# Performance work log

Hardware: AMD Instinct MI355X
Metric: run time of the kernel (lower is better)

Reference implementation:

```python
import jax, jax.numpy as jnp
import numpy as np

B, S, D, H = 4, 2048, 1024, 16
HD = D // H  # head_dim = 64


def setup_inputs() -> dict:
    key = jax.random.key(0)
    ks = jax.random.split(key, 5)
    scale = 0.02
    x = jax.random.normal(ks[0], (B, S, D), dtype=jnp.float32)
    W_qkv = jax.random.normal(ks[1], (D, 3 * D), dtype=jnp.float32) * scale
    b_qkv = jnp.zeros((3 * D,), dtype=jnp.float32)
    W_out = jax.random.normal(ks[2], (D, D), dtype=jnp.float32) * scale
    b_out = jnp.zeros((D,), dtype=jnp.float32)
    return {"x": x, "W_qkv": W_qkv, "b_qkv": b_qkv, "W_out": W_out, "b_out": b_out}


def reference(x, W_qkv, b_qkv, W_out, b_out):
    b, s, d = x.shape
    qkv = x @ W_qkv + b_qkv                      # [B,S,3D]
    q, k, v = jnp.split(qkv, 3, axis=-1)
    # [B,S,D] -> [B,H,S,hd]
    q = q.reshape(b, s, H, HD).transpose(0, 2, 1, 3)
    k = k.reshape(b, s, H, HD).transpose(0, 2, 1, 3)
    v = v.reshape(b, s, H, HD).transpose(0, 2, 1, 3)
    scores = jnp.einsum('bhqd,bhkd->bhqk', q, k) / jnp.sqrt(jnp.float32(HD))
    causal = jnp.tril(jnp.ones((s, s), dtype=bool))  # [S,S]
    scores = jnp.where(causal[None, None], scores, -jnp.inf)
    probs = jax.nn.softmax(scores, axis=-1)
    # dropout is identity in eval mode
    attn = jnp.einsum('bhqk,bhkd->bhqd', probs, v)  # [B,H,S,hd]
    attn = attn.transpose(0, 2, 1, 3).reshape(b, s, d)
    return attn @ W_out + b_out
```

## Files before the change

### kernel.cpp

```cpp
#include <hip/hip_runtime.h>


typedef short s16;
typedef __attribute__((ext_vector_type(4))) short s16x4;
typedef __attribute__((ext_vector_type(8))) short bf16x8;
typedef __attribute__((ext_vector_type(4))) float f32x4;

__device__ __forceinline__ s16 f2bf(float f) {
    union { float f; unsigned int i; } v;
    v.f = f;
    unsigned int r = v.i + 0x7fffu + ((v.i >> 16) & 1u);
    return (s16)(r >> 16);
}

__device__ __forceinline__ void load_lds16(const s16* g, s16* lds_base) {
    __builtin_amdgcn_global_load_lds(
        (const __attribute__((address_space(1))) void*)g,
        (__attribute__((address_space(3))) void*)lds_base, 16, 0, 0);
}

__global__ void cast_f32_bf16(const float* __restrict__ in, s16* __restrict__ out) {
    const int i = (blockIdx.x * 256 + threadIdx.x) * 4;
    const float4 f = *(const float4*)(in + i);
    s16x4 r = {f2bf(f.x), f2bf(f.y), f2bf(f.z), f2bf(f.w)};
    *(s16x4*)(out + i) = r;
}

__global__ void transpose_cast(const float* __restrict__ in,
                               s16* __restrict__ out, int R, int C) {
    __shared__ float tile[32][33];
    const int cb = blockIdx.x * 32, rb = blockIdx.y * 32;
    const int tx = threadIdx.x, ty = threadIdx.y;
#pragma unroll
    for (int i = 0; i < 32; i += 8)
        tile[ty + i][tx] = in[(size_t)(rb + ty + i) * C + cb + tx];
    __syncthreads();
#pragma unroll
    for (int i = 0; i < 32; i += 8)
        out[(size_t)(cb + ty + i) * R + rb + tx] = f2bf(tile[tx][ty + i]);
}

template <bool OUT_F32>
__global__ __launch_bounds__(256) void gemm_bt_bias(
    const s16* __restrict__ A,
    const s16* __restrict__ Bt,
    const float* __restrict__ bias,
    void* __restrict__ Cv,
    int M, int N, int K) {
    __shared__ __attribute__((aligned(16))) s16 As[128 * 32];
    __shared__ __attribute__((aligned(16))) s16 Bs[128 * 32];

    const int tid  = threadIdx.x;
    const int lane = tid & 63;
    const int wave = tid >> 6;
    const int l15  = lane & 15;
    const int quad = lane >> 4;
    const int m0 = blockIdx.y * 128;
    const int n0 = blockIdx.x * 128;
    const int wm = (wave & 1) * 64;
    const int wn = (wave >> 1) * 64;

    f32x4 acc[4][4];
#pragma unroll
    for (int i = 0; i < 4; ++i)
#pragma unroll
        for (int j = 0; j < 4; ++j)
            acc[i][j] = (f32x4){0.f, 0.f, 0.f, 0.f};

    const int r_a = tid >> 2;
    const int kp  = tid & 3;

    for (int k0 = 0; k0 < K; k0 += 32) {
        __syncthreads();
#pragma unroll
        for (int c = 0; c < 2; ++c) {
            load_lds16(A  + (size_t)(m0 + c * 64 + r_a) * K + k0 + kp * 8, As + c * 2048 + wave * 512);
            load_lds16(Bt + (size_t)(n0 + c * 64 + r_a) * K + k0 + kp * 8, Bs + c * 2048 + wave * 512);
        }
        __syncthreads();

        bf16x8 af[4], bfv[4];
#pragma unroll
        for (int mt = 0; mt < 4; ++mt)
            af[mt] = *(const bf16x8*)(As + (wm + mt * 16 + l15) * 32 + quad * 8);
#pragma unroll
        for (int nt = 0; nt < 4; ++nt)
            bfv[nt] = *(const bf16x8*)(Bs + (wn + nt * 16 + l15) * 32 + quad * 8);
#pragma unroll
        for (int mt = 0; mt < 4; ++mt)
#pragma unroll
            for (int nt = 0; nt < 4; ++nt)
                acc[mt][nt] = __builtin_amdgcn_mfma_f32_16x16x32_bf16(af[mt], bfv[nt], acc[mt][nt], 0, 0, 0);
    }

#pragma unroll
    for (int nt = 0; nt < 4; ++nt) {
        const int col = n0 + wn + nt * 16 + l15;
        const float bv = bias[col];
#pragma unroll
        for (int mt = 0; mt < 4; ++mt) {
            const int rowb = m0 + wm + mt * 16 + quad * 4;
#pragma unroll
            for (int r = 0; r < 4; ++r) {
                const float v = acc[mt][nt][r] + bv;
                if constexpr (OUT_F32)
                    ((float*)Cv)[(size_t)(rowb + r) * N + col] = v;
                else
                    ((s16*)Cv)[(size_t)(rowb + r) * N + col] = f2bf(v);
            }
        }
    }
}

__global__ __launch_bounds__(256) void attn_fwd(
    const s16* __restrict__ qkv,
    s16* __restrict__ attn) {
    __shared__ __attribute__((aligned(16))) s16 Ks[64 * 72];
    __shared__ __attribute__((aligned(16))) s16 Vt[64 * 72];
    __shared__ __attribute__((aligned(16))) s16 Ps[4][2][16][72];

    const int tid  = threadIdx.x;
    const int lane = tid & 63;
    const int wave = tid >> 6;
    const int l15  = lane & 15;
    const int quad = lane >> 4;
    const int bh = blockIdx.y;
    const size_t rowbase = (size_t)(bh >> 4) * 2048;
    const int hoff = (bh & 15) * 64;
    const int r_s = tid >> 3;
    const int p_s = tid & 7;

    const float C2 = 0.18033688011112042f;
    const float M2 = 12.0f;

#pragma unroll
    for (int phase = 0; phase < 2; ++phase) {
        const int qt = phase ? 15 - (int)blockIdx.x : (int)blockIdx.x;
        const int qbase = qt * 128;
        const int wq = qbase + wave * 32;

        bf16x8 qf[2][2];
#pragma unroll
        for (int mt = 0; mt < 2; ++mt)
#pragma unroll
            for (int ks = 0; ks < 2; ++ks)
                qf[mt][ks] = *(const bf16x8*)(qkv + (rowbase + wq + mt * 16 + l15) * 3072 + hoff + ks * 32 + quad * 8);

        float l_lane[2][4];
        f32x4 o[2][4];
#pragma unroll
        for (int mt = 0; mt < 2; ++mt) {
#pragma unroll
            for (int r = 0; r < 4; ++r) l_lane[mt][r] = 0.f;
#pragma unroll
            for (int n = 0; n < 4; ++n) o[mt][n] = (f32x4){0.f, 0.f, 0.f, 0.f};
        }

        const int nkt = qt * 2 + 2;
        for (int kt = 0; kt < nkt; ++kt) {
            const int k0 = kt * 64;
            bf16x8 kv[2], vv[2];
#pragma unroll
            for (int c = 0; c < 2; ++c) {
                const s16* g = qkv + (rowbase + k0 + c * 32 + r_s) * 3072 + hoff + p_s * 8;
                kv[c] = *(const bf16x8*)(g + 1024);
                vv[c] = *(const bf16x8*)(g + 2048);
            }
            __syncthreads();
#pragma unroll
            for (int c = 0; c < 2; ++c) {
                const int k = c * 32 + r_s;
                *(bf16x8*)(Ks + k * 72 + p_s * 8) = kv[c];
                const int gsw = (((k >> 3) ^ p_s) << 3) + (k & 7);
#pragma unroll
                for (int j = 0; j < 8; ++j)
                    Vt[(p_s * 8 + j) * 72 + gsw] = vv[c][j];
            }
            __syncthreads();

            if (k0 > wq + 31) continue;

            f32x4 sc[2][4];
#pragma unroll
            for (int mt = 0; mt < 2; ++mt)
#pragma unroll
                for (int nt = 0; nt < 4; ++nt)
                    sc[mt][nt] = (f32x4){0.f, 0.f, 0.f, 0.f};
#pragma unroll
            for (int nt = 0; nt < 4; ++nt)
#pragma unroll
                for (int ks = 0; ks < 2; ++ks) {
                    const bf16x8 kf = *(const bf16x8*)(Ks + (nt * 16 + l15) * 72 + ks * 32 + quad * 8);
#pragma unroll
                    for (int mt = 0; mt < 2; ++mt)
                        sc[mt][nt] = __builtin_amdgcn_mfma_f32_16x16x32_bf16(qf[mt][ks], kf, sc[mt][nt], 0, 0, 0);
                }

            const bool edge = (k0 + 63 > wq);
#pragma unroll
            for (int mt = 0; mt < 2; ++mt)
#pragma unroll
                for (int nt = 0; nt < 4; ++nt) {
                    const int key = k0 + nt * 16 + l15;
#pragma unroll
                    for (int r = 0; r < 4; ++r) {
                        float t = fmaf(sc[mt][nt][r], C2, -M2);
                        if (edge) {
                            const int qrow = wq + mt * 16 + quad * 4 + r;
                            t = (key <= qrow) ? t : -150.f;
                        }
                        const float p = __builtin_amdgcn_exp2f(t);
                        l_lane[mt][r] += p;
                        Ps[wave][mt][quad * 4 + r][nt * 16 + l15] = f2bf(p);
                    }
                }

#pragma unroll
            for (int ks = 0; ks < 2; ++ks) {
                bf16x8 pf[2];
#pragma unroll
                for (int mt = 0; mt < 2; ++mt)
                    pf[mt] = *(const bf16x8*)(&Ps[wave][mt][l15][ks * 32 + quad * 8]);
#pragma unroll
                for (int n = 0; n < 4; ++n) {
                    const bf16x8 vf = *(const bf16x8*)(
                        Vt + (n * 16 + l15) * 72 + (((ks * 4 + quad) ^ (2 * n + (l15 >> 3))) << 3));
#pragma unroll
                    for (int mt = 0; mt < 2; ++mt)
                        o[mt][n] = __builtin_amdgcn_mfma_f32_16x16x32_bf16(pf[mt], vf, o[mt][n], 0, 0, 0);
                }
            }
        }

#pragma unroll
        for (int mt = 0; mt < 2; ++mt)
#pragma unroll
            for (int r = 0; r < 4; ++r) {
#pragma unroll
                for (int d = 1; d < 16; d <<= 1)
                    l_lane[mt][r] += __shfl_xor(l_lane[mt][r], d);
            }

#pragma unroll
        for (int mt = 0; mt < 2; ++mt)
#pragma unroll
            for (int n = 0; n < 4; ++n)
#pragma unroll
                for (int r = 0; r < 4; ++r) {
                    const int qrow = wq + mt * 16 + quad * 4 + r;
                    attn[(rowbase + qrow) * 1024 + hoff + n * 16 + l15] = f2bf(o[mt][n][r] / l_lane[mt][r]);
                }
    }
}

extern "C" void kernel_launch(void* const* d_in, const int* in_sizes, int n_in,
                              void* d_out, int out_size, void* d_ws, size_t ws_size,
                              hipStream_t stream) {
    const float* x    = (const float*)d_in[0];
    const float* Wqkv = (const float*)d_in[1];
    const float* bqkv = (const float*)d_in[2];
    const float* Wout = (const float*)d_in[3];
    const float* bout = (const float*)d_in[4];
    float* out = (float*)d_out;

    s16* ws   = (s16*)d_ws;
    s16* qkv  = ws;
    s16* xba  = qkv + (size_t)8192 * 3072;
    s16* wtq  = xba + (size_t)8192 * 1024;
    s16* wto  = wtq + (size_t)3072 * 1024;

    cast_f32_bf16<<<8192, 256, 0, stream>>>(x, xba);
    transpose_cast<<<dim3(3072 / 32, 1024 / 32), dim3(32, 8), 0, stream>>>(Wqkv, wtq, 1024, 3072);
    transpose_cast<<<dim3(1024 / 32, 1024 / 32), dim3(32, 8), 0, stream>>>(Wout, wto, 1024, 1024);
    gemm_bt_bias<false><<<dim3(3072 / 128, 8192 / 128), 256, 0, stream>>>(
        xba, wtq, bqkv, qkv, 8192, 3072, 1024);
    attn_fwd<<<dim3(8, 64), 256, 0, stream>>>(qkv, xba);
    gemm_bt_bias<true><<<dim3(1024 / 128, 8192 / 128), 256, 0, stream>>>(
        xba, wto, bout, out, 8192, 1024, 1024);
}
```

Measured before the change: 290.6 us.

## Transpose attention MFMA operands, prefetch next K/V tile, vectorize P/V stores

The attention kernel now computes S^T and O^T by swapping the MFMA operands. Each lane then holds four consecutive keys for a single query, so P can be packed into bf16 pairs and written to LDS as 8-byte stores. The row-sum reduction also shrinks to two shuffles, and the output is written as packed uint2. The next K/V tile is loaded into registers during compute, and the V transpose writes dwords instead of single shorts. The intent is fewer LDS and global store instructions and hidden global load latency. The cost is more register pressure, and the rounding changes to round-half-up instead of round-to-nearest-even.

```diff
diff --git a/kernel.cpp b/kernel.cpp
--- a/kernel.cpp
+++ b/kernel.cpp
@@ -11,6 +11,12 @@
     v.f = f;
     unsigned int r = v.i + 0x7fffu + ((v.i >> 16) & 1u);
     return (s16)(r >> 16);
+}
+
+__device__ __forceinline__ unsigned pack_bf16(float a, float b) {
+    union { float f; unsigned u; } x, y;
+    x.f = a; y.f = b;
+    return __byte_perm(x.u + 0x8000u, y.u + 0x8000u, 0x7632);
 }
 
 __device__ __forceinline__ void load_lds16(const s16* g, s16* lds_base) {
@@ -117,7 +123,7 @@
     s16* __restrict__ attn) {
     __shared__ __attribute__((aligned(16))) s16 Ks[64 * 72];
     __shared__ __attribute__((aligned(16))) s16 Vt[64 * 72];
-    __shared__ __attribute__((aligned(16))) s16 Ps[4][2][16][72];
+    __shared__ __attribute__((aligned(16))) s16 PT[4][32][88];
 
     const int tid  = threadIdx.x;
     const int lane = tid & 63;
@@ -127,129 +133,143 @@
     const int bh = blockIdx.y;
     const size_t rowbase = (size_t)(bh >> 4) * 2048;
     const int hoff = (bh & 15) * 64;
-    const int r_s = tid >> 3;
+    const int kp  = tid >> 3;
     const int p_s = tid & 7;
+    const int kg  = kp >> 2;
 
     const float C2 = 0.18033688011112042f;
     const float M2 = 12.0f;
 
-#pragma unroll
     for (int phase = 0; phase < 2; ++phase) {
         const int qt = phase ? 15 - (int)blockIdx.x : (int)blockIdx.x;
-        const int qbase = qt * 128;
-        const int wq = qbase + wave * 32;
+        const int wq = qt * 128 + wave * 32;
 
         bf16x8 qf[2][2];
 #pragma unroll
-        for (int mt = 0; mt < 2; ++mt)
+        for (int qs = 0; qs < 2; ++qs)
 #pragma unroll
             for (int ks = 0; ks < 2; ++ks)
-                qf[mt][ks] = *(const bf16x8*)(qkv + (rowbase + wq + mt * 16 + l15) * 3072 + hoff + ks * 32 + quad * 8);
-
-        float l_lane[2][4];
+                qf[qs][ks] = *(const bf16x8*)(qkv + (rowbase + wq + qs * 16 + l15) * 3072 + hoff + ks * 32 + quad * 8);
+
+        float l_lane[2] = {0.f, 0.f};
         f32x4 o[2][4];
 #pragma unroll
-        for (int mt = 0; mt < 2; ++mt) {
-#pragma unroll
-            for (int r = 0; r < 4; ++r) l_lane[mt][r] = 0.f;
-#pragma unroll
-            for (int n = 0; n < 4; ++n) o[mt][n] = (f32x4){0.f, 0.f, 0.f, 0.f};
-        }
+        for (int qs = 0; qs < 2; ++qs)
+#pragma unroll
+            for (int hs = 0; hs < 4; ++hs)
+                o[qs][hs] = (f32x4){0.f, 0.f, 0.f, 0.f};
 
         const int nkt = qt * 2 + 2;
+        bf16x8 kv[2], vv[2];
+#pragma unroll
+        for (int dk = 0; dk < 2; ++dk) {
+            const s16* g = qkv + (rowbase + 2 * kp + dk) * 3072 + hoff + p_s * 8;
+            kv[dk] = *(const bf16x8*)(g + 1024);
+            vv[dk] = *(const bf16x8*)(g + 2048);
+        }
+
         for (int kt = 0; kt < nkt; ++kt) {
             const int k0 = kt * 64;
-            bf16x8 kv[2], vv[2];
-#pragma unroll
-            for (int c = 0; c < 2; ++c) {
-                const s16* g = qkv + (rowbase + k0 + c * 32 + r_s) * 3072 + hoff + p_s * 8;
-                kv[c] = *(const bf16x8*)(g + 1024);
-                vv[c] = *(const bf16x8*)(g + 2048);
-            }
             __syncthreads();
 #pragma unroll
-            for (int c = 0; c < 2; ++c) {
-                const int k = c * 32 + r_s;
-                *(bf16x8*)(Ks + k * 72 + p_s * 8) = kv[c];
-                const int gsw = (((k >> 3) ^ p_s) << 3) + (k & 7);
-#pragma unroll
-                for (int j = 0; j < 8; ++j)
-                    Vt[(p_s * 8 + j) * 72 + gsw] = vv[c][j];
+            for (int dk = 0; dk < 2; ++dk)
+                *(bf16x8*)(Ks + (2 * kp + dk) * 72 + p_s * 8) = kv[dk];
+#pragma unroll
+            for (int j = 0; j < 8; ++j) {
+                const unsigned dw = (unsigned)(unsigned short)vv[0][j] |
+                                    ((unsigned)(unsigned short)vv[1][j] << 16);
+                *(unsigned*)(Vt + (p_s * 8 + j) * 72 + ((kg ^ p_s) << 3) + (2 * kp & 7)) = dw;
             }
             __syncthreads();
 
+            if (kt + 1 < nkt) {
+#pragma unroll
+                for (int dk = 0; dk < 2; ++dk) {
+                    const s16* g = qkv + (rowbase + k0 + 64 + 2 * kp + dk) * 3072 + hoff + p_s * 8;
+                    kv[dk] = *(const bf16x8*)(g + 1024);
+                    vv[dk] = *(const bf16x8*)(g + 2048);
+                }
+            }
+
             if (k0 > wq + 31) continue;
 
-            f32x4 sc[2][4];
-#pragma unroll
-            for (int mt = 0; mt < 2; ++mt)
-#pragma unroll
-                for (int nt = 0; nt < 4; ++nt)
-                    sc[mt][nt] = (f32x4){0.f, 0.f, 0.f, 0.f};
-#pragma unroll
-            for (int nt = 0; nt < 4; ++nt)
+            f32x4 st[2][4];
+#pragma unroll
+            for (int qs = 0; qs < 2; ++qs)
+#pragma unroll
+                for (int kb = 0; kb < 4; ++kb)
+                    st[qs][kb] = (f32x4){0.f, 0.f, 0.f, 0.f};
+#pragma unroll
+            for (int kb = 0; kb < 4; ++kb)
 #pragma unroll
                 for (int ks = 0; ks < 2; ++ks) {
-                    const bf16x8 kf = *(const bf16x8*)(Ks + (nt * 16 + l15) * 72 + ks * 32 + quad * 8);
-#pragma unroll
-                    for (int mt = 0; mt < 2; ++mt)
-                        sc[mt][nt] = __builtin_amdgcn_mfma_f32_16x16x32_bf16(qf[mt][ks], kf, sc[mt][nt], 0, 0, 0);
+                    const bf16x8 kf = *(const bf16x8*)(Ks + (kb * 16 + l15) * 72 + ks * 32 + quad * 8);
+#pragma unroll
+                    for (int qs = 0; qs < 2; ++qs)
+                        st[qs][kb] = __builtin_amdgcn_mfma_f32_16x16x32_bf16(kf, qf[qs][ks], st[qs][kb], 0, 0, 0);
                 }
 
             const bool edge = (k0 + 63 > wq);
 #pragma unroll
-            for (int mt = 0; mt < 2; ++mt)
-#pragma unroll
-                for (int nt = 0; nt < 4; ++nt) {
-                    const int key = k0 + nt * 16 + l15;
+            for (int qs = 0; qs < 2; ++qs) {
+                const int q = wq + qs * 16 + l15;
+#pragma unroll
+                for (int kb = 0; kb < 4; ++kb) {
+                    float p4[4];
 #pragma unroll
                     for (int r = 0; r < 4; ++r) {
-                        float t = fmaf(sc[mt][nt][r], C2, -M2);
+                        float t = fmaf(st[qs][kb][r], C2, -M2);
                         if (edge) {
-                            const int qrow = wq + mt * 16 + quad * 4 + r;
-                            t = (key <= qrow) ? t : -150.f;
+                            const int key = k0 + kb * 16 + quad * 4 + r;
+                            t = (key <= q) ? t : -150.f;
                         }
-                        const float p = __builtin_amdgcn_exp2f(t);
-                        l_lane[mt][r] += p;
-                        Ps[wave][mt][quad * 4 + r][nt * 16 + l15] = f2bf(p);
+                        p4[r] = __builtin_amdgcn_exp2f(t);
+                        l_lane[qs] += p4[r];
                     }
+                    uint2 dd;
+                    dd.x = pack_bf16(p4[0], p4[1]);
+                    dd.y = pack_bf16(p4[2], p4[3]);
+                    *(uint2*)(&PT[wave][qs * 16 + l15][kb * 16 + quad * 4]) = dd;
                 }
-
-#pragma unroll
-            for (int ks = 0; ks < 2; ++ks) {
+            }
+
+#pragma unroll
+            for (int kk = 0; kk < 2; ++kk) {
                 bf16x8 pf[2];
 #pragma unroll
-                for (int mt = 0; mt < 2; ++mt)
-                    pf[mt] = *(const bf16x8*)(&Ps[wave][mt][l15][ks * 32 + quad * 8]);
-#pragma unroll
-                for (int n = 0; n < 4; ++n) {
+                for (int qs = 0; qs < 2; ++qs)
+                    pf[qs] = *(const bf16x8*)(&PT[wave][qs * 16 + l15][kk * 32 + quad * 8]);
+#pragma unroll
+                for (int hs = 0; hs < 4; ++hs) {
                     const bf16x8 vf = *(const bf16x8*)(
-                        Vt + (n * 16 + l15) * 72 + (((ks * 4 + quad) ^ (2 * n + (l15 >> 3))) << 3));
-#pragma unroll
-                    for (int mt = 0; mt < 2; ++mt)
-                        o[mt][n] = __builtin_amdgcn_mfma_f32_16x16x32_bf16(pf[mt], vf, o[mt][n], 0, 0, 0);
+                        Vt + (hs * 16 + l15) * 72 + (((kk * 4 + quad) ^ (2 * hs + (l15 >> 3))) << 3));
+#pragma unroll
+                    for (int qs = 0; qs < 2; ++qs)
+                        o[qs][hs] = __builtin_amdgcn_mfma_f32_16x16x32_bf16(vf, pf[qs], o[qs][hs], 0, 0, 0);
                 }
             }
         }
 
-#pragma unroll
-        for (int mt = 0; mt < 2; ++mt)
-#pragma unroll
-            for (int r = 0; r < 4; ++r) {
-#pragma unroll
-                for (int d = 1; d < 16; d <<= 1)
-                    l_lane[mt][r] += __shfl_xor(l_lane[mt][r], d);
-            }
-
-#pragma unroll
-        for (int mt = 0; mt < 2; ++mt)
-#pragma unroll
-            for (int n = 0; n < 4; ++n)
-#pragma unroll
-                for (int r = 0; r < 4; ++r) {
-                    const int qrow = wq + mt * 16 + quad * 4 + r;
-                    attn[(rowbase + qrow) * 1024 + hoff + n * 16 + l15] = f2bf(o[mt][n][r] / l_lane[mt][r]);
-                }
+        float rl[2];
+#pragma unroll
+        for (int qs = 0; qs < 2; ++qs) {
+            float l = l_lane[qs];
+            l += __shfl_xor(l, 16);
+            l += __shfl_xor(l, 32);
+            rl[qs] = 1.f / l;
+        }
+
+#pragma unroll
+        for (int qs = 0; qs < 2; ++qs) {
+            const int q = wq + qs * 16 + l15;
+#pragma unroll
+            for (int hs = 0; hs < 4; ++hs) {
+                uint2 dd;
+                dd.x = pack_bf16(o[qs][hs][0] * rl[qs], o[qs][hs][1] * rl[qs]);
+                dd.y = pack_bf16(o[qs][hs][2] * rl[qs], o[qs][hs][3] * rl[qs]);
+                *(uint2*)(attn + (rowbase + q) * 1024 + hoff + hs * 16 + quad * 4) = dd;
+            }
+        }
     }
 }
 
```

After: 278.8 us. 4.1% less time.
